# Kernel optimization log

Hardware: AMD Instinct MI355X
Metric: run time of the kernel (lower is better)

## Reference

```python
import jax, jax.numpy as jnp
import numpy as np

EMBED_DIM = 1024
NUM_HEADS = 16
HEAD_DIM = EMBED_DIM // NUM_HEADS


def setup_inputs() -> dict:
    key = jax.random.key(0)
    ks = jax.random.split(key, 9)
    s = 1.0 / np.sqrt(EMBED_DIM)
    mk = lambda k: jax.random.uniform(k, (EMBED_DIM, EMBED_DIM), jnp.float32, -s, s)
    bk = lambda k: jax.random.uniform(k, (EMBED_DIM,), jnp.float32, -s, s)
    return {
        "input_tensor": jax.random.normal(ks[0], (4, 2048, EMBED_DIM), jnp.float32),
        "wq": mk(ks[1]), "bq": bk(ks[2]),
        "wk": mk(ks[3]), "bk_": bk(ks[4]),
        "wv": mk(ks[5]), "bv": bk(ks[6]),
        "wo": mk(ks[7]), "bo": bk(ks[8]),
    }


def reference(input_tensor, wq, bq, wk, bk_, wv, bv, wo, bo):
    B, S, E = input_tensor.shape
    H, D = NUM_HEADS, HEAD_DIM
    # torch Linear: y = x @ W.T + b
    q = input_tensor @ wq.T + bq
    k = input_tensor @ wk.T + bk_
    v = input_tensor @ wv.T + bv
    q = q.reshape(B, S, H, D).transpose(0, 2, 1, 3)  # [B,H,S,D]
    k = k.reshape(B, S, H, D).transpose(0, 2, 1, 3)
    v = v.reshape(B, S, H, D).transpose(0, 2, 1, 3)
    scores = jnp.einsum('bhsd,bhtd->bhst', q, k) / jnp.sqrt(jnp.float32(D))
    attn = jax.nn.softmax(scores, axis=-1)  # dropout p=0 -> identity
    out = jnp.einsum('bhst,bhtd->bhsd', attn, v)
    out = out.transpose(0, 2, 1, 3).reshape(B, S, E)
    return out @ wo.T + bo
```

## Files before the change

kernel.cpp:

```cpp
#include <hip/hip_runtime.h>

typedef __bf16 bf16x8 __attribute__((ext_vector_type(8)));
typedef float  f32x4  __attribute__((ext_vector_type(4)));
typedef float  f32x16 __attribute__((ext_vector_type(16)));
typedef unsigned u32x4 __attribute__((ext_vector_type(4)));

#define NB 4
#define SEQ 2048
#define EMB 1024
#define NH 16
#define HD 64
#define MTOT (NB * SEQ)

__device__ __forceinline__ unsigned short f2bf(float f) {
    unsigned u = __float_as_uint(f);
    return (unsigned short)((u + 0x7fffu + ((u >> 16) & 1u)) >> 16);
}

__device__ __forceinline__ void gload16(const void* g, void* l) {
    __builtin_amdgcn_global_load_lds(
        (const __attribute__((address_space(1))) unsigned int*)g,
        (__attribute__((address_space(3))) unsigned int*)l,
        16, 0, 0);
}

__global__ __launch_bounds__(256) void cast_all(
    const float* __restrict__ X, const float* __restrict__ a,
    const float* __restrict__ b, const float* __restrict__ c,
    const float* __restrict__ d, unsigned short* __restrict__ oX,
    unsigned short* __restrict__ oa, unsigned short* __restrict__ ob,
    unsigned short* __restrict__ oc, unsigned short* __restrict__ od) {
    int blk = blockIdx.x;
    const float* src;
    unsigned short* dst;
    int i;
    if (blk < 8192) {
        src = X; dst = oX; i = blk * 256 + threadIdx.x;
    } else {
        int wblk = blk - 8192;
        int which = wblk >> 10;
        src = which == 0 ? a : which == 1 ? b : which == 2 ? c : d;
        dst = which == 0 ? oa : which == 1 ? ob : which == 2 ? oc : od;
        i = (wblk & 1023) * 256 + threadIdx.x;
    }
    float4 v = ((const float4*)src)[i];
    ushort4 r;
    r.x = f2bf(v.x); r.y = f2bf(v.y); r.z = f2bf(v.z); r.w = f2bf(v.w);
    ((ushort4*)dst)[i] = r;
}

__global__ __launch_bounds__(256) void gemm_qkv(
    const unsigned short* __restrict__ A, const unsigned short* __restrict__ W3,
    const float* __restrict__ bq, const float* __restrict__ bk,
    const float* __restrict__ bv, unsigned short* __restrict__ Qo,
    unsigned short* __restrict__ Ko, unsigned short* __restrict__ Vto) {
    constexpr int K = EMB;
    __shared__ __align__(16) unsigned short As[128 * 64];
    __shared__ __align__(16) unsigned short Bs[128 * 64];

    const int lane = threadIdx.x & 63;
    const int wv   = threadIdx.x >> 6;
    const int wr   = wv >> 1, wc = wv & 1;
    const int f    = blockIdx.x;
    const int w    = (f & 7) * 192 + (f >> 3);
    const int m0   = (w / 24) * 128, n0 = (w % 24) * 128;
    const int proj = n0 >> 10;
    const float* bp = proj == 0 ? bq : proj == 1 ? bk : bv;
    const float oscale = proj == 0 ? 0.18033688011112043f : 1.0f;

    f32x4 acc[4][4];
#pragma unroll
    for (int a = 0; a < 4; ++a)
#pragma unroll
        for (int b = 0; b < 4; ++b) acc[a][b] = (f32x4){0.f, 0.f, 0.f, 0.f};

    const int gsw = ((lane & 7) ^ (lane >> 3)) * 8;
    for (int kt = 0; kt < K / 64; ++kt) {
        if (kt) __syncthreads();
#pragma unroll
        for (int j = 0; j < 4; ++j) {
            int rb = (wv * 4 + j) * 8;
            int r  = rb + (lane >> 3);
            gload16(A + (size_t)(m0 + r) * K + kt * 64 + gsw, &As[rb * 64]);
            gload16(W3 + (size_t)(n0 + r) * K + kt * 64 + gsw, &Bs[rb * 64]);
        }
        __syncthreads();
#pragma unroll
        for (int ks = 0; ks < 2; ++ks) {
            const int slot = ((ks * 4 + (lane >> 4)) ^ (lane & 7)) * 8;
            bf16x8 af[4], bf_[4];
#pragma unroll
            for (int x = 0; x < 4; ++x) {
                af[x]  = *(const bf16x8*)&As[(wr * 64 + x * 16 + (lane & 15)) * 64 + slot];
                bf_[x] = *(const bf16x8*)&Bs[(wc * 64 + x * 16 + (lane & 15)) * 64 + slot];
            }
#pragma unroll
            for (int mi = 0; mi < 4; ++mi)
#pragma unroll
                for (int ni = 0; ni < 4; ++ni)
                    acc[mi][ni] = __builtin_amdgcn_mfma_f32_16x16x32_bf16(
                        af[mi], bf_[ni], acc[mi][ni], 0, 0, 0);
        }
    }

#pragma unroll
    for (int mi = 0; mi < 4; ++mi) {
#pragma unroll
        for (int ni = 0; ni < 4; ++ni) {
            int n    = n0 + wc * 64 + ni * 16 + (lane & 15);
            int nloc = n & 1023;
            float bvv = bp[nloc];
            int h = nloc >> 6, d = nloc & 63;
#pragma unroll
            for (int i = 0; i < 4; ++i) {
                int m = m0 + wr * 64 + mi * 16 + (lane >> 4) * 4 + i;
                float v = (acc[mi][ni][i] + bvv) * oscale;
                int b = m >> 11, s = m & (SEQ - 1);
                if (proj == 0)
                    Qo[(((size_t)(b * NH + h) * SEQ + s) << 6) + d] = f2bf(v);
                else if (proj == 1)
                    Ko[(((size_t)(b * NH + h) * SEQ + s) << 6) + d] = f2bf(v);
                else
                    Vto[((size_t)(b * NH + h) * 64 + d) * SEQ + s] = f2bf(v);
            }
        }
    }
}

__global__ __launch_bounds__(256) void gemm_out(
    const unsigned short* __restrict__ A, const unsigned short* __restrict__ W,
    const float* __restrict__ bias, float* __restrict__ out) {
    constexpr int K = EMB;
    __shared__ __align__(16) unsigned short As[128 * 64];
    __shared__ __align__(16) unsigned short Bs[128 * 64];

    const int lane = threadIdx.x & 63;
    const int wv   = threadIdx.x >> 6;
    const int wr   = wv >> 1, wc = wv & 1;
    const int f    = blockIdx.x;
    const int w    = (f & 7) * 64 + (f >> 3);
    const int m0   = (w / 8) * 128, n0 = (w % 8) * 128;

    f32x4 acc[4][4];
#pragma unroll
    for (int a = 0; a < 4; ++a)
#pragma unroll
        for (int b = 0; b < 4; ++b) acc[a][b] = (f32x4){0.f, 0.f, 0.f, 0.f};

    const int gsw = ((lane & 7) ^ (lane >> 3)) * 8;
    for (int kt = 0; kt < K / 64; ++kt) {
        if (kt) __syncthreads();
#pragma unroll
        for (int j = 0; j < 4; ++j) {
            int rb = (wv * 4 + j) * 8;
            int r  = rb + (lane >> 3);
            gload16(A + (size_t)(m0 + r) * K + kt * 64 + gsw, &As[rb * 64]);
            gload16(W + (size_t)(n0 + r) * K + kt * 64 + gsw, &Bs[rb * 64]);
        }
        __syncthreads();
#pragma unroll
        for (int ks = 0; ks < 2; ++ks) {
            const int slot = ((ks * 4 + (lane >> 4)) ^ (lane & 7)) * 8;
            bf16x8 af[4], bf_[4];
#pragma unroll
            for (int x = 0; x < 4; ++x) {
                af[x]  = *(const bf16x8*)&As[(wr * 64 + x * 16 + (lane & 15)) * 64 + slot];
                bf_[x] = *(const bf16x8*)&Bs[(wc * 64 + x * 16 + (lane & 15)) * 64 + slot];
            }
#pragma unroll
            for (int mi = 0; mi < 4; ++mi)
#pragma unroll
                for (int ni = 0; ni < 4; ++ni)
                    acc[mi][ni] = __builtin_amdgcn_mfma_f32_16x16x32_bf16(
                        af[mi], bf_[ni], acc[mi][ni], 0, 0, 0);
        }
    }

#pragma unroll
    for (int mi = 0; mi < 4; ++mi) {
#pragma unroll
        for (int ni = 0; ni < 4; ++ni) {
            int n = n0 + wc * 64 + ni * 16 + (lane & 15);
            float bv = bias[n];
#pragma unroll
            for (int i = 0; i < 4; ++i) {
                int m = m0 + wr * 64 + mi * 16 + (lane >> 4) * 4 + i;
                out[(size_t)m * EMB + n] = acc[mi][ni][i] + bv;
            }
        }
    }
}

__global__ __launch_bounds__(512, 4) void attn_fwd(
    const unsigned short* __restrict__ Q, const unsigned short* __restrict__ K,
    const unsigned short* __restrict__ Vt, unsigned short* __restrict__ AO) {
    const int qt = blockIdx.x >> 6;
    const int bh = blockIdx.x & 63;
    const int lane = threadIdx.x & 63;
    const int wv   = threadIdx.x >> 6;
    const int l31  = lane & 31;
    const int lh   = lane >> 5;

    __shared__ __align__(16) unsigned short Ks[2][8 * 64 * 8];
    __shared__ __align__(16) unsigned short Vs[2][8 * 64 * 8];

    const unsigned short* Kb = K + (size_t)bh * SEQ * HD;
    const unsigned short* Vb = Vt + (size_t)bh * HD * SEQ;

    const unsigned short* Qp = Q + ((size_t)bh * SEQ + qt * 256 + wv * 32 + l31) * HD + lh * 8;
    bf16x8 qfr[4];
#pragma unroll
    for (int kc = 0; kc < 4; ++kc) qfr[kc] = *(const bf16x8*)(Qp + kc * 16);

    const u32x4 onesu = {0x3F803F80u, 0x3F803F80u, 0x3F803F80u, 0x3F803F80u};
    const bf16x8 ones = __builtin_bit_cast(bf16x8, onesu);

    f32x16 oT[2], lT;
#pragma unroll
    for (int r = 0; r < 16; ++r) { oT[0][r] = 0.f; oT[1][r] = 0.f; lT[r] = 0.f; }

    auto stageKV = [&](int buf, int t) {
        gload16(Kb + (size_t)(t * 64 + lane) * HD + wv * 8, &Ks[buf][wv * 512]);
        gload16(Vb + (size_t)lane * SEQ + t * 64 + wv * 8, &Vs[buf][wv * 512]);
    };

    stageKV(0, 0);

    for (int t = 0; t < SEQ / 64; ++t) {
        const int cur = t & 1;
        __syncthreads();
        if (t + 1 < SEQ / 64) stageKV(cur ^ 1, t + 1);

#pragma unroll
        for (int sub = 0; sub < 2; ++sub) {
            f32x16 st;
#pragma unroll
            for (int r = 0; r < 16; ++r) st[r] = 0.f;
            const int krow = sub * 32 + l31;
            __builtin_amdgcn_s_setprio(1);
#pragma unroll
            for (int kc = 0; kc < 4; ++kc) {
                bf16x8 kf = *(const bf16x8*)&Ks[cur][(kc * 2 + lh) * 512 + krow * 8];
                st = __builtin_amdgcn_mfma_f32_32x32x16_bf16(kf, qfr[kc], st, 0, 0, 0);
            }
            __builtin_amdgcn_s_setprio(0);

            unsigned w0, w1, w2, w3, w4, w5, w6, w7;
#define EXPPK(WI, RA, RB)                                                     \
            {                                                                 \
                float pa = __builtin_amdgcn_exp2f(st[RA]);                    \
                float pb = __builtin_amdgcn_exp2f(st[RB]);                    \
                asm("v_cvt_pk_bf16_f32 %0, %1, %2" : "=v"(WI) : "v"(pa), "v"(pb)); \
            }
            EXPPK(w0, 0, 1)  EXPPK(w1, 2, 3)  EXPPK(w2, 4, 5)  EXPPK(w3, 6, 7)
            EXPPK(w4, 8, 9)  EXPPK(w5, 10, 11) EXPPK(w6, 12, 13) EXPPK(w7, 14, 15)
#undef EXPPK
            asm volatile("v_permlane32_swap_b32 %0, %1" : "+v"(w0), "+v"(w2));
            asm volatile("v_permlane32_swap_b32 %0, %1" : "+v"(w1), "+v"(w3));
            asm volatile("v_permlane32_swap_b32 %0, %1" : "+v"(w4), "+v"(w6));
            asm volatile("v_permlane32_swap_b32 %0, %1" : "+v"(w5), "+v"(w7));
            u32x4 a0 = {w0, w1, w2, w3};
            u32x4 a1 = {w4, w5, w6, w7};
            bf16x8 pf0 = __builtin_bit_cast(bf16x8, a0);
            bf16x8 pf1 = __builtin_bit_cast(bf16x8, a1);

            __builtin_amdgcn_s_setprio(1);
            lT = __builtin_amdgcn_mfma_f32_32x32x16_bf16(ones, pf0, lT, 0, 0, 0);
            lT = __builtin_amdgcn_mfma_f32_32x32x16_bf16(ones, pf1, lT, 0, 0, 0);
#pragma unroll
            for (int dt = 0; dt < 2; ++dt) {
                int d = dt * 32 + l31;
#pragma unroll
                for (int ks = 0; ks < 2; ++ks) {
                    bf16x8 vf = *(const bf16x8*)&Vs[cur][(sub * 4 + ks * 2 + lh) * 512 + d * 8];
                    oT[dt] = __builtin_amdgcn_mfma_f32_32x32x16_bf16(
                        vf, ks ? pf1 : pf0, oT[dt], 0, 0, 0);
                }
            }
            __builtin_amdgcn_s_setprio(0);
        }
    }

    float inv = 1.0f / lT[0];
    const int b = bh >> 4, h = bh & 15;
    const int q = qt * 256 + wv * 32 + l31;
    unsigned short* aor = AO + (((size_t)b * SEQ + q) * NH + h) * HD;
#pragma unroll
    for (int dt = 0; dt < 2; ++dt) {
#pragma unroll
        for (int g = 0; g < 4; ++g) {
            ushort4 o;
            o.x = f2bf(oT[dt][g * 4 + 0] * inv);
            o.y = f2bf(oT[dt][g * 4 + 1] * inv);
            o.z = f2bf(oT[dt][g * 4 + 2] * inv);
            o.w = f2bf(oT[dt][g * 4 + 3] * inv);
            *(ushort4*)(aor + dt * 32 + g * 8 + lh * 4) = o;
        }
    }
}

extern "C" void kernel_launch(void* const* d_in, const int* in_sizes, int n_in,
                              void* d_out, int out_size, void* d_ws, size_t ws_size,
                              hipStream_t stream) {
    const float* X  = (const float*)d_in[0];
    const float* wq = (const float*)d_in[1];
    const float* bq = (const float*)d_in[2];
    const float* wk = (const float*)d_in[3];
    const float* bk = (const float*)d_in[4];
    const float* wv = (const float*)d_in[5];
    const float* bv = (const float*)d_in[6];
    const float* wo = (const float*)d_in[7];
    const float* bo = (const float*)d_in[8];
    float* out = (float*)d_out;

    unsigned short* ws = (unsigned short*)d_ws;
    const size_t XE = (size_t)MTOT * EMB;
    const size_t WE = (size_t)EMB * EMB;
    unsigned short* Xb  = ws;
    unsigned short* Wqb = ws + XE;
    unsigned short* Wkb = Wqb + WE;
    unsigned short* Wvb = Wkb + WE;
    unsigned short* Wob = Wvb + WE;
    unsigned short* Qb  = Wob + WE;
    unsigned short* Kb  = Qb + XE;
    unsigned short* Vtb = Kb + XE;
    unsigned short* AOb = Xb;

    cast_all<<<12288, 256, 0, stream>>>(X, wq, wk, wv, wo, Xb, Wqb, Wkb, Wvb, Wob);

    gemm_qkv<<<1536, 256, 0, stream>>>(Xb, Wqb, bq, bk, bv, Qb, Kb, Vtb);

    attn_fwd<<<512, 512, 0, stream>>>(Qb, Kb, Vtb, AOb);

    gemm_out<<<512, 256, 0, stream>>>(AOb, Wob, bo, out);
}
```

Baseline: 182.4 us.

## Double-buffer LDS in projection GEMMs with k-grouped layout and MFMA priority

Both projection GEMMs (QKV and output) now use two LDS buffers with a K-tile of 32, so the async global-to-LDS load of the next tile is issued before computing on the current one. The LDS layout changes from a swizzled row-major 64-wide tile to a k-group-major layout where each 8-element chunk group is stored contiguously. The MFMA block is wrapped in s_setprio to favour the math waves. This trades a halved K tile (twice as many barriers) for overlap of memory latency with compute, and the new layout may introduce different LDS bank behaviour.

```diff
diff --git a/kernel.cpp b/kernel.cpp
--- a/kernel.cpp
+++ b/kernel.cpp
@@ -55,8 +55,9 @@
     const float* __restrict__ bv, unsigned short* __restrict__ Qo,
     unsigned short* __restrict__ Ko, unsigned short* __restrict__ Vto) {
     constexpr int K = EMB;
-    __shared__ __align__(16) unsigned short As[128 * 64];
-    __shared__ __align__(16) unsigned short Bs[128 * 64];
+    constexpr int NT = K / 32;
+    __shared__ __align__(16) unsigned short As[2][4096];
+    __shared__ __align__(16) unsigned short Bs[2][4096];
 
     const int lane = threadIdx.x & 63;
     const int wv   = threadIdx.x >> 6;
@@ -74,33 +75,41 @@
 #pragma unroll
         for (int b = 0; b < 4; ++b) acc[a][b] = (f32x4){0.f, 0.f, 0.f, 0.f};
 
-    const int gsw = ((lane & 7) ^ (lane >> 3)) * 8;
-    for (int kt = 0; kt < K / 64; ++kt) {
-        if (kt) __syncthreads();
-#pragma unroll
-        for (int j = 0; j < 4; ++j) {
-            int rb = (wv * 4 + j) * 8;
-            int r  = rb + (lane >> 3);
-            gload16(A + (size_t)(m0 + r) * K + kt * 64 + gsw, &As[rb * 64]);
-            gload16(W3 + (size_t)(n0 + r) * K + kt * 64 + gsw, &Bs[rb * 64]);
-        }
+    auto stage = [&](int buf, int kt) {
+#pragma unroll
+        for (int j = 0; j < 2; ++j) {
+            int s = wv * 2 + j, g = s & 3, half = s >> 2;
+            gload16(A + (size_t)(m0 + half * 64 + lane) * K + kt * 32 + g * 8,
+                    &As[buf][g * 1024 + half * 512]);
+            gload16(W3 + (size_t)(n0 + half * 64 + lane) * K + kt * 32 + g * 8,
+                    &Bs[buf][g * 1024 + half * 512]);
+        }
+    };
+
+    auto compute = [&](int cur) {
+        const int gfr = lane >> 4;
+        bf16x8 af[4], bfr[4];
+#pragma unroll
+        for (int x = 0; x < 4; ++x) {
+            af[x]  = *(const bf16x8*)&As[cur][gfr * 1024 + (wr * 64 + x * 16 + (lane & 15)) * 8];
+            bfr[x] = *(const bf16x8*)&Bs[cur][gfr * 1024 + (wc * 64 + x * 16 + (lane & 15)) * 8];
+        }
+        __builtin_amdgcn_s_setprio(1);
+#pragma unroll
+        for (int mi = 0; mi < 4; ++mi)
+#pragma unroll
+            for (int ni = 0; ni < 4; ++ni)
+                acc[mi][ni] = __builtin_amdgcn_mfma_f32_16x16x32_bf16(
+                    af[mi], bfr[ni], acc[mi][ni], 0, 0, 0);
+        __builtin_amdgcn_s_setprio(0);
+    };
+
+    stage(0, 0);
+    for (int kt = 0; kt < NT; ++kt) {
+        const int cur = kt & 1;
         __syncthreads();
-#pragma unroll
-        for (int ks = 0; ks < 2; ++ks) {
-            const int slot = ((ks * 4 + (lane >> 4)) ^ (lane & 7)) * 8;
-            bf16x8 af[4], bf_[4];
-#pragma unroll
-            for (int x = 0; x < 4; ++x) {
-                af[x]  = *(const bf16x8*)&As[(wr * 64 + x * 16 + (lane & 15)) * 64 + slot];
-                bf_[x] = *(const bf16x8*)&Bs[(wc * 64 + x * 16 + (lane & 15)) * 64 + slot];
-            }
-#pragma unroll
-            for (int mi = 0; mi < 4; ++mi)
-#pragma unroll
-                for (int ni = 0; ni < 4; ++ni)
-                    acc[mi][ni] = __builtin_amdgcn_mfma_f32_16x16x32_bf16(
-                        af[mi], bf_[ni], acc[mi][ni], 0, 0, 0);
-        }
+        if (kt + 1 < NT) stage(cur ^ 1, kt + 1);
+        compute(cur);
     }
 
 #pragma unroll
@@ -131,8 +140,9 @@
     const unsigned short* __restrict__ A, const unsigned short* __restrict__ W,
     const float* __restrict__ bias, float* __restrict__ out) {
     constexpr int K = EMB;
-    __shared__ __align__(16) unsigned short As[128 * 64];
-    __shared__ __align__(16) unsigned short Bs[128 * 64];
+    constexpr int NT = K / 32;
+    __shared__ __align__(16) unsigned short As[2][4096];
+    __shared__ __align__(16) unsigned short Bs[2][4096];
 
     const int lane = threadIdx.x & 63;
     const int wv   = threadIdx.x >> 6;
@@ -147,33 +157,41 @@
 #pragma unroll
         for (int b = 0; b < 4; ++b) acc[a][b] = (f32x4){0.f, 0.f, 0.f, 0.f};
 
-    const int gsw = ((lane & 7) ^ (lane >> 3)) * 8;
-    for (int kt = 0; kt < K / 64; ++kt) {
-        if (kt) __syncthreads();
-#pragma unroll
-        for (int j = 0; j < 4; ++j) {
-            int rb = (wv * 4 + j) * 8;
-            int r  = rb + (lane >> 3);
-            gload16(A + (size_t)(m0 + r) * K + kt * 64 + gsw, &As[rb * 64]);
-            gload16(W + (size_t)(n0 + r) * K + kt * 64 + gsw, &Bs[rb * 64]);
-        }
+    auto stage = [&](int buf, int kt) {
+#pragma unroll
+        for (int j = 0; j < 2; ++j) {
+            int s = wv * 2 + j, g = s & 3, half = s >> 2;
+            gload16(A + (size_t)(m0 + half * 64 + lane) * K + kt * 32 + g * 8,
+                    &As[buf][g * 1024 + half * 512]);
+            gload16(W + (size_t)(n0 + half * 64 + lane) * K + kt * 32 + g * 8,
+                    &Bs[buf][g * 1024 + half * 512]);
+        }
+    };
+
+    auto compute = [&](int cur) {
+        const int gfr = lane >> 4;
+        bf16x8 af[4], bfr[4];
+#pragma unroll
+        for (int x = 0; x < 4; ++x) {
+            af[x]  = *(const bf16x8*)&As[cur][gfr * 1024 + (wr * 64 + x * 16 + (lane & 15)) * 8];
+            bfr[x] = *(const bf16x8*)&Bs[cur][gfr * 1024 + (wc * 64 + x * 16 + (lane & 15)) * 8];
+        }
+        __builtin_amdgcn_s_setprio(1);
+#pragma unroll
+        for (int mi = 0; mi < 4; ++mi)
+#pragma unroll
+            for (int ni = 0; ni < 4; ++ni)
+                acc[mi][ni] = __builtin_amdgcn_mfma_f32_16x16x32_bf16(
+                    af[mi], bfr[ni], acc[mi][ni], 0, 0, 0);
+        __builtin_amdgcn_s_setprio(0);
+    };
+
+    stage(0, 0);
+    for (int kt = 0; kt < NT; ++kt) {
+        const int cur = kt & 1;
         __syncthreads();
-#pragma unroll
-        for (int ks = 0; ks < 2; ++ks) {
-            const int slot = ((ks * 4 + (lane >> 4)) ^ (lane & 7)) * 8;
-            bf16x8 af[4], bf_[4];
-#pragma unroll
-            for (int x = 0; x < 4; ++x) {
-                af[x]  = *(const bf16x8*)&As[(wr * 64 + x * 16 + (lane & 15)) * 64 + slot];
-                bf_[x] = *(const bf16x8*)&Bs[(wc * 64 + x * 16 + (lane & 15)) * 64 + slot];
-            }
-#pragma unroll
-            for (int mi = 0; mi < 4; ++mi)
-#pragma unroll
-                for (int ni = 0; ni < 4; ++ni)
-                    acc[mi][ni] = __builtin_amdgcn_mfma_f32_16x16x32_bf16(
-                        af[mi], bf_[ni], acc[mi][ni], 0, 0, 0);
-        }
+        if (kt + 1 < NT) stage(cur ^ 1, kt + 1);
+        compute(cur);
     }
 
 #pragma unroll
```

Result: slower. 260.3 us (+42.7%).
